# Optimization experiments

Hardware: AMD Instinct MI355X
Metric: run time of the kernel (lower is better)

The kernel has to match this reference:

```python
import jax, jax.numpy as jnp
import numpy as np

T0 = 0.0
T1 = 20.0
DT0 = 0.02
NT = 1000
N = 64
K = 8
N_ITS = 2


def _lininterp(tg, yg, t):
    # linear interpolation of grid values yg (len(tg), ...) at scalar t
    i = jnp.clip(jnp.searchsorted(tg, t, side='right') - 1, 0, tg.shape[0] - 2)
    w = jnp.clip((t - tg[i]) / (tg[i + 1] - tg[i]), 0.0, 1.0)
    return (1.0 - w) * yg[i] + w * yg[i + 1]


def _rk4(field, y0, t_start, dt, nsteps):
    # fixed-step RK4; returns trajectory of shape (nsteps+1, *y0.shape)
    def step(y, t):
        k1 = field(t, y)
        k2 = field(t + 0.5 * dt, y + 0.5 * dt * k1)
        k3 = field(t + 0.5 * dt, y + 0.5 * dt * k2)
        k4 = field(t + dt, y + dt * k3)
        y1 = y + (dt / 6.0) * (k1 + 2.0 * k2 + 2.0 * k3 + k4)
        return y1, y1
    tgrid = t_start + dt * jnp.arange(nsteps, dtype=y0.dtype)
    _, ys = jax.lax.scan(step, y0, tgrid)
    return jnp.concatenate([y0[None], ys], axis=0)


def setup_inputs() -> dict:
    key = jax.random.key(0)
    ks = jax.random.split(key, 5)
    n, k = N, K
    s = 1.0 / np.sqrt(n)
    A = 0.3 * s * jax.random.normal(ks[0], (n, n), jnp.float32) - 0.5 * jnp.eye(n, dtype=jnp.float32)
    B = s * jax.random.normal(ks[1], (n, k), jnp.float32)
    H = 0.1 * s * jax.random.normal(ks[2], (n, n, k), jnp.float32)
    Rm = jax.random.normal(ks[3], (k, k), jnp.float32)
    R = jnp.eye(k, dtype=jnp.float32) + 0.1 * (Rm @ Rm.T) / k
    Q = jnp.eye(n, dtype=jnp.float32)
    F = 0.5 * jnp.eye(n, dtype=jnp.float32)
    x0 = 0.5 * jax.random.normal(ks[4], (n, 1), jnp.float32)
    return {"F": F, "Q": Q, "R": R, "A": A, "B": B, "H": H, "x0": x0, "N_its": N_ITS}


def _solve(F, Q, R, A, B, H, x0, N_its):
    Ri = jnp.linalg.inv(R)
    dA = jnp.conj(A).T
    ts = T0 + DT0 * jnp.arange(NT, dtype=x0.dtype)              # state grid (excludes t1)
    tgP = T0 + DT0 * jnp.arange(NT + 1, dtype=x0.dtype)         # costate grid (includes t1)

    def A_k_tilde(pk):
        return A - 0.5 * (jnp.einsum('ijk,kl,ml,m->ij', H, Ri, B, pk)
                          + jnp.einsum('ir,rs,mjs,m->ij', B, Ri, H, pk))

    def B_k_tilde(xk):
        return B + jnp.einsum('jnl,n->jl', H, xk)

    def S_k_tilde(xk):
        Bt = B_k_tilde(xk)
        return (jnp.einsum('ik,kl,jl->ij', Bt, Ri, Bt)
                - 0.5 * (jnp.einsum('iqp,q,pr,jr->ij', H, xk, Ri, B)
                         + jnp.einsum('it,tv,jwv,w->ij', B, Ri, H, xk)))

    def Q_k_tilde(pk):
        return (jnp.einsum('m,mik,kl,njl,n->ij', pk, H, Ri, H, pk)
                + jnp.einsum('m,mjr,rs,nis,n->ij', pk, H, Ri, H, pk))

    def A_k(xk, pk, Pk):
        return A_k_tilde(pk) - S_k_tilde(xk) @ Pk

    def Q_k(xk, pk, Pk):
        return Q_k_tilde(pk) - Pk @ S_k_tilde(xk) @ Pk

    def u_k(xk, xk1, Pk1):
        return jnp.einsum('kl,jnl,n,jm,m->k', -Ri, H, xk, Pk1, xk1)

    # LQR Riccati, integrated backward from t1 with y(t1) = F
    def P_field(t, y):
        return -y @ A - dA @ y - Q + jnp.einsum('im,mk,kl,nl,nj->ij', y, B, Ri, B, y)
    Ps = jnp.flip(_rk4(P_field, F, T1, -DT0, NT), axis=0)        # (NT+1, n, n) on tgP
    P_of = lambda t: _lininterp(tgP, Ps, t)

    x_res = jnp.zeros((N_its + 1, NT, N), dtype=x0.dtype)
    u_res = jnp.zeros((N_its + 1, NT, K), dtype=x0.dtype)

    # iteration 0: no control
    x0_traj = _rk4(lambda t, y: A @ y, x0, T0, DT0, NT - 1)       # (NT, n, 1)
    x_res = x_res.at[0].set(x0_traj[:, :, 0])

    # iteration 1: LQR initial guess
    def init_field(t, y):
        return (A - jnp.einsum('ik,kl,nl,nj->ij', B, Ri, B, P_of(t))) @ y
    x_grid = _rk4(init_field, x0, T0, DT0, NT - 1)                # (NT, n, 1)
    x_res = x_res.at[1].set(x_grid[:, :, 0])
    u1 = jax.vmap(lambda Pt, xt: -jnp.einsum('kl,nl,nj,j->k', Ri, B, Pt, xt))(Ps[:NT], x_grid[:, :, 0])
    u_res = u_res.at[1].set(u1)

    P_grid = Ps
    for i in range(1, N_its):
        x_of = lambda t, xg=x_grid: _lininterp(ts, xg, t)[:, 0]
        Pc_of = lambda t, Pg=P_grid: _lininterp(tgP, Pg, t)

        def Akt_field(t, y, x_of=x_of, Pc_of=Pc_of):
            Pkt = Pc_of(t)
            xkt = x_of(t)
            pkt = Pkt @ xkt
            return A_k(xkt, pkt, Pkt) @ y

        x_k1 = _rk4(Akt_field, x0, T0, DT0, NT - 1)               # (NT, n, 1)

        def Pk1_field(t, y, x_of=x_of, Pc_of=Pc_of):
            Pkt = Pc_of(t)
            xkt = x_of(t)
            pkt = Pkt @ xkt
            Akt = A_k(xkt, pkt, Pkt)
            return -y @ Akt - Akt.T @ y - Q_k(xkt, pkt, Pkt)

        P_k1 = jnp.flip(_rk4(Pk1_field, F, T1, -DT0, NT), axis=0)  # (NT+1, n, n)

        u_grid = jax.vmap(u_k)(x_grid[:, :, 0], x_k1[:, :, 0], P_k1[:NT])  # (NT, k)
        u_of = lambda t, ug=u_grid: _lininterp(ts, ug, t)

        def eval_field(t, y, x_of=x_of, Pc_of=Pc_of, u_of=u_of):
            xkt = x_of(t)
            pkt = Pc_of(t) @ xkt
            return A_k_tilde(pkt) @ y + (B_k_tilde(xkt) @ u_of(t))[:, None]

        x_eval = _rk4(eval_field, x0, T0, DT0, NT - 1)            # (NT, n, 1)
        x_res = x_res.at[i + 1].set(x_eval[:, :, 0])
        u_res = u_res.at[i + 1].set(u_grid)
        x_grid = x_k1
        P_grid = P_k1
    return x_res, u_res


def reference(F, Q, R, A, B, H, x0, N_its):
    return _solve(F, Q, R, A, B, H, x0, int(N_its))
```

## Files before the change

kernel.cpp:

```cpp
#include <hip/hip_runtime.h>
#include <cmath>


#define NTS 1000
#define DT  0.02f
#define LDM 68

constexpr int O_PS   = 0;
constexpr int O_PK1  = O_PS  + (NTS+1)*4096;
constexpr int O_XG   = O_PK1 + NTS*4096;
constexpr int O_XK1  = O_XG  + NTS*64;
constexpr int O_H1   = O_XK1 + NTS*64;
constexpr int O_H2   = O_H1  + 64*8*64;
constexpr int O_RI   = O_H2  + 64*8*64;
constexpr int O_BRI  = O_RI  + 64;
constexpr int O_RIBT = O_BRI + 512;
constexpr int O_BT   = O_RIBT+ 512;
constexpr int WS_FLOATS = O_BT + 512;

constexpr int O_X0o = 0;
constexpr int O_X1o = 64000;
constexpr int O_X2o = 128000;
constexpr int O_U0o = 192000;
constexpr int O_U1o = 200000;
constexpr int O_U2o = 208000;

#define EW_FOR(I, J, IJ, ...) do { \
  const int _r = (int)threadIdx.x >> 2; const int _c0 = ((int)threadIdx.x & 3) << 4; \
  _Pragma("unroll") \
  for (int _e = 0; _e < 16; ++_e) { const int I = _r; const int J = _c0 + _e; const int IJ = (I)*LDM + (J); __VA_ARGS__; } \
} while (0)

__device__ __forceinline__ void ld4(float* d, const float* p) {
  const float4 v = *(const float4*)p; d[0]=v.x; d[1]=v.y; d[2]=v.z; d[3]=v.w;
}

template<int KD, int LDX, int LDY, int LDC, int OP>
__device__ __forceinline__ void mmNN(float* C, const float* X, const float* Y) {
  const int t = threadIdx.x;
  const int ti = (t >> 4) << 2, tj = (t & 15) << 2;
  float c[4][4] = {};
  #pragma unroll
  for (int m = 0; m < KD; m += 4) {
    float xv[4][4], yv[4][4];
    #pragma unroll
    for (int r = 0; r < 4; ++r) ld4(xv[r], &X[(ti + r) * LDX + m]);
    #pragma unroll
    for (int k = 0; k < 4; ++k) ld4(yv[k], &Y[(m + k) * LDY + tj]);
    #pragma unroll
    for (int r = 0; r < 4; ++r)
      #pragma unroll
      for (int k = 0; k < 4; ++k)
        #pragma unroll
        for (int j = 0; j < 4; ++j) c[r][j] += xv[r][k] * yv[k][j];
  }
  #pragma unroll
  for (int r = 0; r < 4; ++r) {
    float* dst = &C[(ti + r) * LDC + tj];
    #pragma unroll
    for (int j = 0; j < 4; ++j) {
      if (OP == 0) dst[j] = c[r][j];
      else if (OP == 1) dst[j] += c[r][j];
      else dst[j] -= c[r][j];
    }
  }
}

template<int KD, int LDX, int LDY, int LDC, int OP>
__device__ __forceinline__ void mmTN(float* C, const float* X, const float* Y) {
  const int t = threadIdx.x;
  const int ti = (t >> 4) << 2, tj = (t & 15) << 2;
  float c[4][4] = {};
  #pragma unroll
  for (int m = 0; m < KD; m += 4) {
    float xq[4][4], yv[4][4];
    #pragma unroll
    for (int k = 0; k < 4; ++k) ld4(xq[k], &X[(m + k) * LDX + ti]);
    #pragma unroll
    for (int k = 0; k < 4; ++k) ld4(yv[k], &Y[(m + k) * LDY + tj]);
    #pragma unroll
    for (int r = 0; r < 4; ++r)
      #pragma unroll
      for (int k = 0; k < 4; ++k)
        #pragma unroll
        for (int j = 0; j < 4; ++j) c[r][j] += xq[k][r] * yv[k][j];
  }
  #pragma unroll
  for (int r = 0; r < 4; ++r) {
    float* dst = &C[(ti + r) * LDC + tj];
    #pragma unroll
    for (int j = 0; j < 4; ++j) {
      if (OP == 0) dst[j] = c[r][j];
      else if (OP == 1) dst[j] += c[r][j];
      else dst[j] -= c[r][j];
    }
  }
}

template<int KD, int LDX, int LDYT, int LDC, int OP>
__device__ __forceinline__ void mmNT(float* C, const float* X, const float* Yt) {
  const int t = threadIdx.x;
  const int ti = (t >> 4) << 2, tj = (t & 15) << 2;
  float c[4][4] = {};
  #pragma unroll
  for (int m = 0; m < KD; m += 4) {
    float xv[4][4], yq[4][4];
    #pragma unroll
    for (int r = 0; r < 4; ++r) ld4(xv[r], &X[(ti + r) * LDX + m]);
    #pragma unroll
    for (int cc = 0; cc < 4; ++cc) ld4(yq[cc], &Yt[(tj + cc) * LDYT + m]);
    #pragma unroll
    for (int r = 0; r < 4; ++r)
      #pragma unroll
      for (int k = 0; k < 4; ++k)
        #pragma unroll
        for (int j = 0; j < 4; ++j) c[r][j] += xv[r][k] * yq[j][k];
  }
  #pragma unroll
  for (int r = 0; r < 4; ++r) {
    float* dst = &C[(ti + r) * LDC + tj];
    #pragma unroll
    for (int j = 0; j < 4; ++j) {
      if (OP == 0) dst[j] = c[r][j];
      else if (OP == 1) dst[j] += c[r][j];
      else dst[j] -= c[r][j];
    }
  }
}

__device__ __forceinline__ void mv64(float* out, const float* M, int ldm, const float* v, float* red) {
  const int t = threadIdx.x;
  const int r = t & 63, q = t >> 6, m0 = q << 4;
  float s = 0.f;
  #pragma unroll
  for (int m = 0; m < 16; ++m) s += M[r*ldm + m0 + m] * v[m0 + m];
  red[(q << 6) + r] = s;
  __syncthreads();
  if (t < 64) out[t] = (red[t] + red[64+t]) + (red[128+t] + red[192+t]);
  __syncthreads();
}

__device__ __forceinline__ void mv64_blend(float* out, const float* Ma, const float* Mb,
                                           float wa, float wb, const float* v, float* red) {
  const int t = threadIdx.x;
  const int r = t & 63, q = t >> 6, m0 = q << 4;
  float sa = 0.f, sb = 0.f;
  #pragma unroll
  for (int m = 0; m < 16; ++m) {
    const float vv = v[m0 + m];
    sa += Ma[r*64 + m0 + m] * vv;
    sb += Mb[r*64 + m0 + m] * vv;
  }
  red[(q << 6) + r] = wa*sa + wb*sb;
  __syncthreads();
  if (t < 64) out[t] = (red[t] + red[64+t]) + (red[128+t] + red[192+t]);
  __syncthreads();
}

__device__ __forceinline__ float dot64g(const float* __restrict__ a, const float* v) {
  float s = 0.f;
  #pragma unroll
  for (int m = 0; m < 64; m += 4) {
    const float4 av = *(const float4*)&a[m];
    s += av.x*v[m] + av.y*v[m+1] + av.z*v[m+2] + av.w*v[m+3];
  }
  return s;
}

__device__ __forceinline__ void interpIW(float t, int imax, int& i, float& w) {
  int ii = (int)floorf(t * 50.0f);
  ii = ii < 0 ? 0 : (ii > imax ? imax : ii);
  const float gi  = DT * (float)ii;
  const float gi1 = DT * (float)(ii + 1);
  float ww = (t - gi) / (gi1 - gi);
  ww = fminf(fmaxf(ww, 0.0f), 1.0f);
  i = ii; w = ww;
}

__global__ void kPrepA(const float* __restrict__ Rg, const float* __restrict__ Bg, float* __restrict__ ws) {
  __shared__ float M[8][17];
  __shared__ int spiv;
  const int t = threadIdx.x;
  if (t < 8) {
    #pragma unroll
    for (int c = 0; c < 8; ++c) { M[t][c] = Rg[t*8 + c]; M[t][8 + c] = (t == c) ? 1.0f : 0.0f; }
  }
  __syncthreads();
  for (int col = 0; col < 8; ++col) {
    if (t == 0) {
      int piv = col; float best = fabsf(M[col][col]);
      for (int r = col + 1; r < 8; ++r) { const float a = fabsf(M[r][col]); if (a > best) { best = a; piv = r; } }
      spiv = piv;
    }
    __syncthreads();
    const int piv = spiv;
    if (piv != col && t < 16) { const float tmp = M[col][t]; M[col][t] = M[piv][t]; M[piv][t] = tmp; }
    __syncthreads();
    if (t < 16) { const float pv = M[col][col]; M[col][t] = M[col][t] / pv; }
    __syncthreads();
    if (t < 8 && t != col) {
      const float f = M[t][col];
      #pragma unroll
      for (int c = 0; c < 16; ++c) M[t][c] -= f * M[col][c];
    }
    __syncthreads();
  }
  if (t < 64) ws[O_RI + t] = M[t >> 3][8 + (t & 7)];
  __syncthreads();
  for (int o = t; o < 512; o += 64) {
    const int i = o >> 3, l = o & 7;
    float s = 0.f;
    #pragma unroll
    for (int p = 0; p < 8; ++p) s += Bg[i*8 + p] * M[p][8 + l];
    ws[O_BRI + o] = s;
    const int p2 = o >> 6, j2 = o & 63;
    float s2 = 0.f;
    #pragma unroll
    for (int l2 = 0; l2 < 8; ++l2) s2 += M[p2][8 + l2] * Bg[j2*8 + l2];
    ws[O_RIBT + o] = s2;
    ws[O_BT + o] = Bg[j2*8 + p2];
  }
}

__global__ void kPrepB(const float* __restrict__ Hg, float* __restrict__ ws, float* __restrict__ out) {
  const int total = 32768 + 32768 + 8000;
  for (int idx = blockIdx.x * 256 + threadIdx.x; idx < total; idx += gridDim.x * 256) {
    if (idx < 32768) {
      const int j = idx >> 9, l = (idx >> 6) & 7, n = idx & 63;
      ws[O_H1 + idx] = Hg[j*512 + n*8 + l];
    } else if (idx < 65536) {
      const int k2 = idx - 32768;
      const int j = k2 >> 9, s = (k2 >> 6) & 7, m = k2 & 63;
      ws[O_H2 + k2] = Hg[m*512 + j*8 + s];
    } else {
      out[O_U0o + (idx - 65536)] = 0.0f;
    }
  }
}

__global__ void __launch_bounds__(256) kP(const float* __restrict__ Fg, const float* __restrict__ Qg,
                                          const float* __restrict__ Ag,
                                          const float* __restrict__ ws, float* __restrict__ Ps) {
  __shared__ float y0[64*LDM], acc[64*LDM], ytm[64*LDM], kb[64*LDM];
  __shared__ float As[64*LDM], ATs[64*LDM], Qs[64*LDM];
  __shared__ float BTs[512], Ris[64], yB[512], M2s[512], T8[8*LDM], red[256];
  const int t = threadIdx.x;
  { const int r = t >> 2, c0 = (t & 3) << 4;
    #pragma unroll
    for (int e = 0; e < 16; ++e) { const int c = c0 + e;
      y0[r*LDM + c]  = Fg[r*64 + c];
      As[r*LDM + c]  = Ag[r*64 + c];
      ATs[c*LDM + r] = Ag[r*64 + c];
      Qs[r*LDM + c]  = Qg[r*64 + c];
    } }
  for (int o = t; o < 512; o += 256) BTs[o] = ws[O_BT + o];
  if (t < 64) Ris[t] = ws[O_RI + t];
  __syncthreads();
  { const int r = t >> 2, c0 = (t & 3) << 4;
    #pragma unroll
    for (int e = 0; e < 16; ++e) Ps[(size_t)NTS*4096 + r*64 + c0 + e] = y0[r*LDM + c0 + e]; }

  const float dt = -DT;
  const float c16 = dt / 6.0f, c13 = 2.0f * c16, c12 = 0.5f * dt;

  auto field = [&](const float* src) {
    for (int o = t; o < 512; o += 256) {
      const int i = o >> 3, l = o & 7;
      const float* sr = &src[i*LDM];
      const float* br = &BTs[l*64];
      float s = 0.f;
      #pragma unroll
      for (int m = 0; m < 64; ++m) s += sr[m] * br[m];
      yB[o] = s;
    }
    __syncthreads();
    for (int o = t; o < 512; o += 256) {
      const int i = o >> 3, l = o & 7;
      float s = 0.f;
      #pragma unroll
      for (int p = 0; p < 8; ++p) s += yB[i*8 + p] * Ris[p*8 + l];
      M2s[o] = s;
    }
    for (int o = t; o < 512; o += 256) {
      const int p = o >> 6, jj = o & 63;
      const float* br = &BTs[p*64];
      float s = 0.f;
      #pragma unroll
      for (int m = 0; m < 64; ++m) s += br[m] * src[m*LDM + jj];
      T8[p*LDM + jj] = s;
    }
    __syncthreads();
    mmNN<8,  8,   LDM, LDM, 0>(kb, M2s, T8);
    mmNN<64, LDM, LDM, LDM, 2>(kb, src, As);
    mmNN<64, LDM, LDM, LDM, 2>(kb, ATs, src);
    __syncthreads();
  };

  for (int j = 0; j < NTS; ++j) {
    for (int st = 0; st < 4; ++st) {
      const float* src = (st == 0) ? y0 : ytm;
      field(src);
      EW_FOR(I, J, IJ, {
        const float kv = kb[IJ] - Qs[IJ];
        if (st == 0)      { acc[IJ] = y0[IJ] + c16*kv; ytm[IJ] = y0[IJ] + c12*kv; }
        else if (st == 1) { acc[IJ] += c13*kv;         ytm[IJ] = y0[IJ] + c12*kv; }
        else if (st == 2) { acc[IJ] += c13*kv;         ytm[IJ] = y0[IJ] + dt*kv;  }
        else              { y0[IJ] = acc[IJ] + c16*kv; }
      });
      __syncthreads();
    }
    { const int r = t >> 2, c0 = (t & 3) << 4;
      float4* dst = (float4*)&Ps[(size_t)(NTS-1-j)*4096 + r*64 + c0];
      #pragma unroll
      for (int e = 0; e < 4; ++e) {
        const float* s4 = &y0[r*LDM + c0 + 4*e];
        dst[e] = make_float4(s4[0], s4[1], s4[2], s4[3]);
      } }
    __syncthreads();
  }
}

__global__ void __launch_bounds__(256) kX0(const float* __restrict__ Ag, const float* __restrict__ x0g,
                                           float* __restrict__ out) {
  __shared__ float As[64*LDM], xv[64], xt[64], ks[4][64], red[256];
  const int t = threadIdx.x;
  { const int r = t >> 2, c0 = (t & 3) << 4;
    #pragma unroll
    for (int e = 0; e < 16; ++e) As[r*LDM + c0 + e] = Ag[r*64 + c0 + e]; }
  if (t < 64) xv[t] = x0g[t];
  __syncthreads();
  for (int j = 0; j < NTS; ++j) {
    if (t < 64) out[O_X0o + j*64 + t] = xv[t];
    __syncthreads();
    if (j == NTS - 1) break;
    for (int st = 0; st < 4; ++st) {
      const float* src = (st == 0) ? xv : xt;
      mv64(ks[st], As, LDM, src, red);
      if (t < 64 && st < 3) xt[t] = xv[t] + (st == 2 ? DT : 0.01f) * ks[st][t];
      __syncthreads();
    }
    if (t < 64) xv[t] += (DT/6.0f) * (ks[0][t] + 2.0f*ks[1][t] + 2.0f*ks[2][t] + ks[3][t]);
    __syncthreads();
  }
}

__global__ void __launch_bounds__(256) kXgrid(const float* __restrict__ Ag, const float* __restrict__ Bg,
                                              const float* __restrict__ x0g,
                                              float* __restrict__ ws, float* __restrict__ out) {
  __shared__ float As[64*LDM], Bs[512], RiBTs[512];
  __shared__ float xv[64], xt[64], ks[4][64], pv[64], g8[8], red[256];
  const int t = threadIdx.x;
  const float* Ps = ws + O_PS;
  { const int r = t >> 2, c0 = (t & 3) << 4;
    #pragma unroll
    for (int e = 0; e < 16; ++e) As[r*LDM + c0 + e] = Ag[r*64 + c0 + e]; }
  for (int o = t; o < 512; o += 256) { Bs[o] = Bg[o]; RiBTs[o] = ws[O_RIBT + o]; }
  if (t < 64) xv[t] = x0g[t];
  __syncthreads();

  auto field = [&](float tau, const float* src, float* kout) {
    int i; float w; interpIW(tau, NTS - 1, i, w);
    mv64_blend(pv, Ps + (size_t)i*4096, Ps + (size_t)(i+1)*4096, 1.0f - w, w, src, red);
    if (t < 8) {
      float s = 0.f;
      #pragma unroll
      for (int m = 0; m < 64; ++m) s += RiBTs[t*64 + m] * pv[m];
      g8[t] = s;
    }
    mv64(kout, As, LDM, src, red);
    if (t < 64) {
      float s = 0.f;
      #pragma unroll
      for (int p = 0; p < 8; ++p) s += Bs[t*8 + p] * g8[p];
      kout[t] -= s;
    }
    __syncthreads();
  };

  for (int j = 0; j < NTS; ++j) {
    if (t < 64) { out[O_X1o + j*64 + t] = xv[t]; ws[O_XG + j*64 + t] = xv[t]; }
    mv64(pv, Ps + (size_t)j*4096, 64, xv, red);
    if (t < 8) {
      float s = 0.f;
      #pragma unroll
      for (int m = 0; m < 64; ++m) s += RiBTs[t*64 + m] * pv[m];
      out[O_U1o + j*8 + t] = -s;
    }
    __syncthreads();
    if (j == NTS - 1) break;
    const float tj = DT * (float)j;
    for (int st = 0; st < 4; ++st) {
      const float tau = tj + ((st == 0) ? 0.0f : (st == 3) ? DT : 0.01f);
      const float* src = (st == 0) ? xv : xt;
      field(tau, src, ks[st]);
      if (t < 64 && st < 3) xt[t] = xv[t] + (st == 2 ? DT : 0.01f) * ks[st][t];
      __syncthreads();
    }
    if (t < 64) xv[t] += (DT/6.0f) * (ks[0][t] + 2.0f*ks[1][t] + 2.0f*ks[2][t] + ks[3][t]);
    __syncthreads();
  }
}

__global__ void __launch_bounds__(256) kXk1(const float* __restrict__ Ag, const float* __restrict__ Bg,
                                            const float* __restrict__ Hg, const float* __restrict__ x0g,
                                            float* __restrict__ ws) {
  __shared__ float Atil[64*LDM];
  __shared__ float Bs[512], BTs[512], RiBTs[512], BRis[512], Ris[64];
  __shared__ float Hx[512], Bt[512], BtRi[512], G[512];
  __shared__ float xv[64], xt[64], xk[64], pk[64], pv[64], sv[64];
  __shared__ float ks[4][64], e1[8], e2[8], e3[8], e8v[8], w8[8], red[256];
  __shared__ int ci; __shared__ float cw;
  const int t = threadIdx.x;
  const float* Ps = ws + O_PS;
  const float* xg = ws + O_XG;
  for (int o = t; o < 512; o += 256) {
    Bs[o] = Bg[o]; BTs[o] = ws[O_BT + o]; RiBTs[o] = ws[O_RIBT + o]; BRis[o] = ws[O_BRI + o];
  }
  if (t < 64) { Ris[t] = ws[O_RI + t]; xv[t] = x0g[t]; }
  __syncthreads();

  auto build = [&](float tau) {
    int i, ix; float w, wx;
    interpIW(tau, NTS - 1, i, w);
    interpIW(tau, NTS - 2, ix, wx);
    if (t == 0) { ci = i; cw = w; }
    if (t < 64) xk[t] = (1.0f - wx) * xg[ix*64 + t] + wx * xg[(ix+1)*64 + t];
    __syncthreads();
    mv64_blend(pk, Ps + (size_t)i*4096, Ps + (size_t)(i+1)*4096, 1.0f - w, w, xk, red);
    if (t < 8) {
      float s = 0.f;
      #pragma unroll
      for (int m = 0; m < 64; ++m) s += BTs[t*64 + m] * pk[m];
      e8v[t] = s;
    }
    __syncthreads();
    if (t < 8) {
      float s = 0.f;
      #pragma unroll
      for (int l = 0; l < 8; ++l) s += Ris[t*8 + l] * e8v[l];
      w8[t] = s;
    }
    for (int o = t; o < 512; o += 256) {
      const float hx = dot64g(&ws[O_H1 + o*64], xk);
      Hx[o] = hx; Bt[o] = Bs[o] + hx;
      G[o]  = dot64g(&ws[O_H2 + o*64], pk);
    }
    __syncthreads();
    for (int o = t; o < 512; o += 256) {
      const int i2 = o >> 3, l = o & 7;
      float s = 0.f;
      #pragma unroll
      for (int p = 0; p < 8; ++p) s += Bt[i2*8 + p] * Ris[p*8 + l];
      BtRi[o] = s;
    }
    EW_FOR(I, J, IJ, {
      const float4 h0 = *(const float4*)&Hg[I*512 + J*8];
      const float4 h1 = *(const float4*)&Hg[I*512 + J*8 + 4];
      Atil[IJ] = h0.x*w8[0]+h0.y*w8[1]+h0.z*w8[2]+h0.w*w8[3]
               + h1.x*w8[4]+h1.y*w8[5]+h1.z*w8[6]+h1.w*w8[7];
    });
    __syncthreads();
    mmNT<8, 8, 8, LDM, 1>(Atil, BRis, G);
    __syncthreads();
    EW_FOR(I, J, IJ, { Atil[IJ] = Ag[I*64 + J] - 0.5f*Atil[IJ]; });
    __syncthreads();
  };

  auto fieldK = [&](const float* src, float* kout) {
    mv64_blend(pv, Ps + (size_t)ci*4096, Ps + (size_t)(ci+1)*4096, 1.0f - cw, cw, src, red);
    if (t < 8) {
      float s = 0.f;
      #pragma unroll
      for (int m = 0; m < 64; ++m) s += Bt[m*8 + t] * pv[m];
      e1[t] = s;
    } else if (t < 16) {
      const int l = t - 8; float s = 0.f;
      #pragma unroll
      for (int m = 0; m < 64; ++m) s += RiBTs[l*64 + m] * pv[m];
      e2[l] = s;
    } else if (t < 24) {
      const int l = t - 16; float s = 0.f;
      #pragma unroll
      for (int m = 0; m < 64; ++m) s += Hx[m*8 + l] * pv[m];
      e3[l] = s;
    }
    __syncthreads();
    if (t < 64) {
      float s1 = 0.f, s2 = 0.f, s3 = 0.f;
      #pragma unroll
      for (int p = 0; p < 8; ++p) {
        s1 += BtRi[t*8 + p] * e1[p];
        s2 += Hx[t*8 + p]   * e2[p];
        s3 += BRis[t*8 + p] * e3[p];
      }
      sv[t] = s1 - 0.5f*(s2 + s3);
    }
    mv64(kout, Atil, LDM, src, red);
    if (t < 64) kout[t] -= sv[t];
    __syncthreads();
  };

  for (int j = 0; j < NTS; ++j) {
    if (t < 64) ws[O_XK1 + j*64 + t] = xv[t];
    __syncthreads();
    if (j == NTS - 1) break;
    const float tj = DT * (float)j;
    for (int st = 0; st < 4; ++st) {
      if (st != 2) build(tj + ((st == 0) ? 0.0f : (st == 3) ? DT : 0.01f));
      const float* src = (st == 0) ? xv : xt;
      fieldK(src, ks[st]);
      if (t < 64 && st < 3) xt[t] = xv[t] + (st == 2 ? DT : 0.01f) * ks[st][t];
      __syncthreads();
    }
    if (t < 64) xv[t] += (DT/6.0f) * (ks[0][t] + 2.0f*ks[1][t] + 2.0f*ks[2][t] + ks[3][t]);
    __syncthreads();
  }
}

__global__ void __launch_bounds__(256) kPk1(const float* __restrict__ Fg, const float* __restrict__ Ag,
                                            const float* __restrict__ Bg, const float* __restrict__ Hg,
                                            float* __restrict__ ws) {
  __shared__ float y0[64*LDM], acc[64*LDM], ytm[64*LDM], kb[64*LDM];
  __shared__ float Pc[64*LDM], Ss[64*LDM], SP[64*LDM], Akt[64*LDM];
  __shared__ float Bs[512], BTs[512], RiBTs[512], BRis[512], Ris[64];
  __shared__ float Hx[512], Bt[512], BtRi[512], G[512], GRi[512];
  __shared__ float xk[64], pk[64], e8v[8], w8[8], red[256];
  const int t = threadIdx.x;
  const float* Ps = ws + O_PS;
  const float* xg = ws + O_XG;
  float* Pk1g = ws + O_PK1;
  { const int r = t >> 2, c0 = (t & 3) << 4;
    #pragma unroll
    for (int e = 0; e < 16; ++e) y0[r*LDM + c0 + e] = Fg[r*64 + c0 + e]; }
  for (int o = t; o < 512; o += 256) {
    Bs[o] = Bg[o]; BTs[o] = ws[O_BT + o]; RiBTs[o] = ws[O_RIBT + o]; BRis[o] = ws[O_BRI + o];
  }
  if (t < 64) Ris[t] = ws[O_RI + t];
  __syncthreads();

  const float dt = -DT;
  const float c16 = dt / 6.0f, c13 = 2.0f * c16, c12 = 0.5f * dt;

  auto build = [&](float tau) {
    int i, ix; float w, wx;
    interpIW(tau, NTS - 1, i, w);
    interpIW(tau, NTS - 2, ix, wx);
    if (t < 64) xk[t] = (1.0f - wx) * xg[ix*64 + t] + wx * xg[(ix+1)*64 + t];
    { const int r = t >> 2, c0 = (t & 3) << 4;
      const float4* pa = (const float4*)&Ps[(size_t)i*4096 + r*64 + c0];
      const float4* pb = (const float4*)&Ps[(size_t)(i+1)*4096 + r*64 + c0];
      const float wa = 1.0f - w;
      #pragma unroll
      for (int e = 0; e < 4; ++e) {
        const float4 a = pa[e], b = pb[e];
        float* d = &Pc[r*LDM + c0 + 4*e];
        d[0] = wa*a.x + w*b.x; d[1] = wa*a.y + w*b.y; d[2] = wa*a.z + w*b.z; d[3] = wa*a.w + w*b.w;
      } }
    __syncthreads();
    mv64(pk, Pc, LDM, xk, red);
    if (t < 8) {
      float s = 0.f;
      #pragma unroll
      for (int m = 0; m < 64; ++m) s += BTs[t*64 + m] * pk[m];
      e8v[t] = s;
    }
    __syncthreads();
    if (t < 8) {
      float s = 0.f;
      #pragma unroll
      for (int l = 0; l < 8; ++l) s += Ris[t*8 + l] * e8v[l];
      w8[t] = s;
    }
    for (int o = t; o < 512; o += 256) {
      const float hx = dot64g(&ws[O_H1 + o*64], xk);
      Hx[o] = hx; Bt[o] = Bs[o] + hx;
      G[o]  = dot64g(&ws[O_H2 + o*64], pk);
    }
    __syncthreads();
    for (int o = t; o < 512; o += 256) {
      const int i2 = o >> 3, l = o & 7;
      float s1 = 0.f, s2 = 0.f;
      #pragma unroll
      for (int p = 0; p < 8; ++p) { s1 += Bt[i2*8 + p] * Ris[p*8 + l]; s2 += G[i2*8 + p] * Ris[p*8 + l]; }
      BtRi[o] = s1; GRi[o] = s2;
    }
    __syncthreads();
    mmNN<8, 8, 64, LDM, 0>(kb, Hx, RiBTs);
    mmNT<8, 8, 8,  LDM, 0>(Ss, BtRi, Bt);
    __syncthreads();
    EW_FOR(I, J, IJ, { Ss[IJ] = Ss[IJ] - 0.5f*(kb[IJ] + kb[J*LDM + I]); });
    __syncthreads();
    mmNN<64, LDM, LDM, LDM, 0>(SP, Ss, Pc);
    __syncthreads();
    mmNN<64, LDM, LDM, LDM, 0>(kb, Pc, SP);
    mmNT<8, 8, 8, LDM, 0>(Ss, GRi, G);
    __syncthreads();
    EW_FOR(I, J, IJ, {
      Pc[IJ] = Ss[IJ] + Ss[J*LDM + I] - kb[IJ];
      const float4 h0 = *(const float4*)&Hg[I*512 + J*8];
      const float4 h1 = *(const float4*)&Hg[I*512 + J*8 + 4];
      Akt[IJ] = h0.x*w8[0]+h0.y*w8[1]+h0.z*w8[2]+h0.w*w8[3]
              + h1.x*w8[4]+h1.y*w8[5]+h1.z*w8[6]+h1.w*w8[7];
    });
    __syncthreads();
    mmNT<8, 8, 8, LDM, 1>(Akt, BRis, G);
    __syncthreads();
    EW_FOR(I, J, IJ, { Akt[IJ] = Ag[I*64 + J] - 0.5f*Akt[IJ] - SP[IJ]; });
    __syncthreads();
  };

  auto evalf = [&](const float* src) {
    mmNN<64, LDM, LDM, LDM, 0>(kb, src, Akt);
    mmTN<64, LDM, LDM, LDM, 1>(kb, Akt, src);
    __syncthreads();
  };

  for (int j = 0; j < NTS; ++j) {
    const float tj = 20.0f - DT * (float)j;
    for (int st = 0; st < 4; ++st) {
      if (st != 2) build(tj - ((st == 0) ? 0.0f : (st == 3) ? DT : 0.01f));
      const float* src = (st == 0) ? y0 : ytm;
      evalf(src);
      EW_FOR(I, J, IJ, {
        const float kv = -(kb[IJ] + Pc[IJ]);
        if (st == 0)      { acc[IJ] = y0[IJ] + c16*kv; ytm[IJ] = y0[IJ] + c12*kv; }
        else if (st == 1) { acc[IJ] += c13*kv;         ytm[IJ] = y0[IJ] + c12*kv; }
        else if (st == 2) { acc[IJ] += c13*kv;         ytm[IJ] = y0[IJ] + dt*kv;  }
        else              { y0[IJ] = acc[IJ] + c16*kv; }
      });
      __syncthreads();
    }
    { const int r = t >> 2, c0 = (t & 3) << 4;
      float4* dst = (float4*)&Pk1g[(size_t)(NTS-1-j)*4096 + r*64 + c0];
      #pragma unroll
      for (int e = 0; e < 4; ++e) {
        const float* s4 = &y0[r*LDM + c0 + 4*e];
        dst[e] = make_float4(s4[0], s4[1], s4[2], s4[3]);
      } }
    __syncthreads();
  }
}

__global__ void __launch_bounds__(256) kUgrid(const float* __restrict__ ws, float* __restrict__ out) {
  const int j = blockIdx.x, t = threadIdx.x;
  __shared__ float xvj[64], x1[64], vv[64], hxv[512], w8s[8], Ris[64], red[256];
  if (t < 64) { xvj[t] = ws[O_XG + j*64 + t]; x1[t] = ws[O_XK1 + j*64 + t]; Ris[t] = ws[O_RI + t]; }
  __syncthreads();
  mv64(vv, ws + O_PK1 + (size_t)j*4096, 64, x1, red);
  for (int o = t; o < 512; o += 256) {
    const int j2 = o >> 3;
    hxv[o] = vv[j2] * dot64g(&ws[O_H1 + o*64], xvj);
  }
  __syncthreads();
  if (t < 8) {
    float s = 0.f;
    #pragma unroll
    for (int j2 = 0; j2 < 64; ++j2) s += hxv[j2*8 + t];
    w8s[t] = s;
  }
  __syncthreads();
  if (t < 8) {
    float s = 0.f;
    #pragma unroll
    for (int l = 0; l < 8; ++l) s += Ris[t*8 + l] * w8s[l];
    out[O_U2o + j*8 + t] = -s;
  }
}

__global__ void __launch_bounds__(256) kXeval(const float* __restrict__ Ag, const float* __restrict__ Bg,
                                              const float* __restrict__ Hg, const float* __restrict__ x0g,
                                              float* __restrict__ ws, float* __restrict__ out) {
  __shared__ float Atil[64*LDM];
  __shared__ float Bs[512], BTs[512], BRis[512], Ris[64];
  __shared__ float Hx[512], Bt[512], G[512];
  __shared__ float xv[64], xt[64], xk[64], pk[64], bu[64];
  __shared__ float ks[4][64], e8v[8], w8[8], uu8[8], red[256];
  const int t = threadIdx.x;
  const float* Ps = ws + O_PS;
  const float* xg = ws + O_XG;
  const float* Ug = out + O_U2o;
  for (int o = t; o < 512; o += 256) { Bs[o] = Bg[o]; BTs[o] = ws[O_BT + o]; BRis[o] = ws[O_BRI + o]; }
  if (t < 64) { Ris[t] = ws[O_RI + t]; xv[t] = x0g[t]; }
  __syncthreads();

  auto build = [&](float tau) {
    int i, ix; float w, wx;
    interpIW(tau, NTS - 1, i, w);
    interpIW(tau, NTS - 2, ix, wx);
    if (t < 64) xk[t] = (1.0f - wx) * xg[ix*64 + t] + wx * xg[(ix+1)*64 + t];
    __syncthreads();
    mv64_blend(pk, Ps + (size_t)i*4096, Ps + (size_t)(i+1)*4096, 1.0f - w, w, xk, red);
    if (t < 8) {
      float s = 0.f;
      #pragma unroll
      for (int m = 0; m < 64; ++m) s += BTs[t*64 + m] * pk[m];
      e8v[t] = s;
    }
    __syncthreads();
    if (t < 8) {
      float s = 0.f;
      #pragma unroll
      for (int l = 0; l < 8; ++l) s += Ris[t*8 + l] * e8v[l];
      w8[t] = s;
    }
    for (int o = t; o < 512; o += 256) {
      const float hx = dot64g(&ws[O_H1 + o*64], xk);
      Hx[o] = hx; Bt[o] = Bs[o] + hx;
      G[o]  = dot64g(&ws[O_H2 + o*64], pk);
    }
    __syncthreads();
    EW_FOR(I, J, IJ, {
      const float4 h0 = *(const float4*)&Hg[I*512 + J*8];
      const float4 h1 = *(const float4*)&Hg[I*512 + J*8 + 4];
      Atil[IJ] = h0.x*w8[0]+h0.y*w8[1]+h0.z*w8[2]+h0.w*w8[3]
               + h1.x*w8[4]+h1.y*w8[5]+h1.z*w8[6]+h1.w*w8[7];
    });
    __syncthreads();
    mmNT<8, 8, 8, LDM, 1>(Atil, BRis, G);
    __syncthreads();
    EW_FOR(I, J, IJ, { Atil[IJ] = Ag[I*64 + J] - 0.5f*Atil[IJ]; });
    if (t < 8) uu8[t] = (1.0f - wx) * Ug[ix*8 + t] + wx * Ug[(ix+1)*8 + t];
    __syncthreads();
    if (t < 64) {
      float s = 0.f;
      #pragma unroll
      for (int l = 0; l < 8; ++l) s += Bt[t*8 + l] * uu8[l];
      bu[t] = s;
    }
    __syncthreads();
  };

  auto fieldE = [&](const float* src, float* kout) {
    mv64(kout, Atil, LDM, src, red);
    if (t < 64) kout[t] += bu[t];
    __syncthreads();
  };

  for (int j = 0; j < NTS; ++j) {
    if (t < 64) out[O_X2o + j*64 + t] = xv[t];
    __syncthreads();
    if (j == NTS - 1) break;
    const float tj = DT * (float)j;
    for (int st = 0; st < 4; ++st) {
      if (st != 2) build(tj + ((st == 0) ? 0.0f : (st == 3) ? DT : 0.01f));
      const float* src = (st == 0) ? xv : xt;
      fieldE(src, ks[st]);
      if (t < 64 && st < 3) xt[t] = xv[t] + (st == 2 ? DT : 0.01f) * ks[st][t];
      __syncthreads();
    }
    if (t < 64) xv[t] += (DT/6.0f) * (ks[0][t] + 2.0f*ks[1][t] + 2.0f*ks[2][t] + ks[3][t]);
    __syncthreads();
  }
}

extern "C" void kernel_launch(void* const* d_in, const int* in_sizes, int n_in,
                              void* d_out, int out_size, void* d_ws, size_t ws_size,
                              hipStream_t stream) {
  const float* F  = (const float*)d_in[0];
  const float* Q  = (const float*)d_in[1];
  const float* R  = (const float*)d_in[2];
  const float* A  = (const float*)d_in[3];
  const float* B  = (const float*)d_in[4];
  const float* H  = (const float*)d_in[5];
  const float* x0 = (const float*)d_in[6];
  float* out = (float*)d_out;
  float* ws  = (float*)d_ws;
  (void)in_sizes; (void)n_in; (void)out_size; (void)ws_size;

  kPrepA<<<1, 64, 0, stream>>>(R, B, ws);
  kPrepB<<<96, 256, 0, stream>>>(H, ws, out);
  kP<<<1, 256, 0, stream>>>(F, Q, A, ws, ws + O_PS);
  kX0<<<1, 256, 0, stream>>>(A, x0, out);
  kXgrid<<<1, 256, 0, stream>>>(A, B, x0, ws, out);
  kXk1<<<1, 256, 0, stream>>>(A, B, H, x0, ws);
  kPk1<<<1, 256, 0, stream>>>(F, A, B, H, ws);
  kUgrid<<<NTS, 256, 0, stream>>>(ws, out);
  kXeval<<<1, 256, 0, stream>>>(A, B, H, x0, ws, out);
}
```

Before: 229.5 ms.

## Widen sequential RK4 kernels to 1024 threads and exploit symmetry in Riccati fields

```diff
diff --git a/kernel.cpp b/kernel.cpp
--- a/kernel.cpp
+++ b/kernel.cpp
@@ -10,13 +10,11 @@
 constexpr int O_PK1  = O_PS  + (NTS+1)*4096;
 constexpr int O_XG   = O_PK1 + NTS*4096;
 constexpr int O_XK1  = O_XG  + NTS*64;
-constexpr int O_H1   = O_XK1 + NTS*64;
-constexpr int O_H2   = O_H1  + 64*8*64;
-constexpr int O_RI   = O_H2  + 64*8*64;
+constexpr int O_H1T  = O_XK1 + NTS*64;
+constexpr int O_RI   = O_H1T + 64*512;
 constexpr int O_BRI  = O_RI  + 64;
 constexpr int O_RIBT = O_BRI + 512;
 constexpr int O_BT   = O_RIBT+ 512;
-constexpr int WS_FLOATS = O_BT + 512;
 
 constexpr int O_X0o = 0;
 constexpr int O_X1o = 64000;
@@ -25,146 +23,134 @@
 constexpr int O_U1o = 200000;
 constexpr int O_U2o = 208000;
 
-#define EW_FOR(I, J, IJ, ...) do { \
-  const int _r = (int)threadIdx.x >> 2; const int _c0 = ((int)threadIdx.x & 3) << 4; \
+#define EW4(I, J, IJ, ...) do { \
+  const int _r = (int)threadIdx.x >> 4; const int _c0 = ((int)threadIdx.x & 15) << 2; \
   _Pragma("unroll") \
-  for (int _e = 0; _e < 16; ++_e) { const int I = _r; const int J = _c0 + _e; const int IJ = (I)*LDM + (J); __VA_ARGS__; } \
+  for (int _e = 0; _e < 4; ++_e) { const int I = _r; const int J = _c0 + _e; const int IJ = (I)*LDM + (J); __VA_ARGS__; } \
 } while (0)
 
-__device__ __forceinline__ void ld4(float* d, const float* p) {
-  const float4 v = *(const float4*)p; d[0]=v.x; d[1]=v.y; d[2]=v.z; d[3]=v.w;
+__device__ __forceinline__ float wred64(float v) {
+  v += __shfl_down(v, 32, 64);
+  v += __shfl_down(v, 16, 64);
+  v += __shfl_down(v, 8, 64);
+  v += __shfl_down(v, 4, 64);
+  v += __shfl_down(v, 2, 64);
+  v += __shfl_down(v, 1, 64);
+  return v;
 }
 
 template<int KD, int LDX, int LDY, int LDC, int OP>
 __device__ __forceinline__ void mmNN(float* C, const float* X, const float* Y) {
   const int t = threadIdx.x;
-  const int ti = (t >> 4) << 2, tj = (t & 15) << 2;
-  float c[4][4] = {};
+  const int row = t >> 4, tj = (t & 15) << 2;
+  float c0 = 0.f, c1 = 0.f, c2 = 0.f, c3 = 0.f;
   #pragma unroll
   for (int m = 0; m < KD; m += 4) {
-    float xv[4][4], yv[4][4];
-    #pragma unroll
-    for (int r = 0; r < 4; ++r) ld4(xv[r], &X[(ti + r) * LDX + m]);
-    #pragma unroll
-    for (int k = 0; k < 4; ++k) ld4(yv[k], &Y[(m + k) * LDY + tj]);
-    #pragma unroll
-    for (int r = 0; r < 4; ++r)
-      #pragma unroll
-      for (int k = 0; k < 4; ++k)
-        #pragma unroll
-        for (int j = 0; j < 4; ++j) c[r][j] += xv[r][k] * yv[k][j];
-  }
-  #pragma unroll
-  for (int r = 0; r < 4; ++r) {
-    float* dst = &C[(ti + r) * LDC + tj];
-    #pragma unroll
-    for (int j = 0; j < 4; ++j) {
-      if (OP == 0) dst[j] = c[r][j];
-      else if (OP == 1) dst[j] += c[r][j];
-      else dst[j] -= c[r][j];
-    }
-  }
-}
-
-template<int KD, int LDX, int LDY, int LDC, int OP>
-__device__ __forceinline__ void mmTN(float* C, const float* X, const float* Y) {
-  const int t = threadIdx.x;
-  const int ti = (t >> 4) << 2, tj = (t & 15) << 2;
-  float c[4][4] = {};
+    const float4 x4 = *(const float4*)&X[row*LDX + m];
+    const float4 ya = *(const float4*)&Y[(m+0)*LDY + tj];
+    const float4 yb = *(const float4*)&Y[(m+1)*LDY + tj];
+    const float4 yc = *(const float4*)&Y[(m+2)*LDY + tj];
+    const float4 yd = *(const float4*)&Y[(m+3)*LDY + tj];
+    c0 += x4.x*ya.x + x4.y*yb.x + x4.z*yc.x + x4.w*yd.x;
+    c1 += x4.x*ya.y + x4.y*yb.y + x4.z*yc.y + x4.w*yd.y;
+    c2 += x4.x*ya.z + x4.y*yb.z + x4.z*yc.z + x4.w*yd.z;
+    c3 += x4.x*ya.w + x4.y*yb.w + x4.z*yc.w + x4.w*yd.w;
+  }
+  float* dst = &C[row*LDC + tj];
+  if (OP == 0)      { dst[0] = c0; dst[1] = c1; dst[2] = c2; dst[3] = c3; }
+  else if (OP == 1) { dst[0] += c0; dst[1] += c1; dst[2] += c2; dst[3] += c3; }
+  else              { dst[0] -= c0; dst[1] -= c1; dst[2] -= c2; dst[3] -= c3; }
+}
+
+template<int KD, int LDX, int LDYT, int LDC, int OP>
+__device__ __forceinline__ void mmNT(float* C, const float* X, const float* Yt) {
+  const int t = threadIdx.x;
+  const int row = t >> 4, tj = (t & 15) << 2;
+  float c[4] = {0.f, 0.f, 0.f, 0.f};
   #pragma unroll
   for (int m = 0; m < KD; m += 4) {
-    float xq[4][4], yv[4][4];
-    #pragma unroll
-    for (int k = 0; k < 4; ++k) ld4(xq[k], &X[(m + k) * LDX + ti]);
-    #pragma unroll
-    for (int k = 0; k < 4; ++k) ld4(yv[k], &Y[(m + k) * LDY + tj]);
-    #pragma unroll
-    for (int r = 0; r < 4; ++r)
-      #pragma unroll
-      for (int k = 0; k < 4; ++k)
-        #pragma unroll
-        for (int j = 0; j < 4; ++j) c[r][j] += xq[k][r] * yv[k][j];
-  }
+    const float4 x4 = *(const float4*)&X[row*LDX + m];
+    #pragma unroll
+    for (int j = 0; j < 4; ++j) {
+      const float4 y4 = *(const float4*)&Yt[(tj+j)*LDYT + m];
+      c[j] += x4.x*y4.x + x4.y*y4.y + x4.z*y4.z + x4.w*y4.w;
+    }
+  }
+  float* dst = &C[row*LDC + tj];
   #pragma unroll
-  for (int r = 0; r < 4; ++r) {
-    float* dst = &C[(ti + r) * LDC + tj];
-    #pragma unroll
-    for (int j = 0; j < 4; ++j) {
-      if (OP == 0) dst[j] = c[r][j];
-      else if (OP == 1) dst[j] += c[r][j];
-      else dst[j] -= c[r][j];
-    }
-  }
-}
-
-template<int KD, int LDX, int LDYT, int LDC, int OP>
-__device__ __forceinline__ void mmNT(float* C, const float* X, const float* Yt) {
-  const int t = threadIdx.x;
-  const int ti = (t >> 4) << 2, tj = (t & 15) << 2;
-  float c[4][4] = {};
-  #pragma unroll
-  for (int m = 0; m < KD; m += 4) {
-    float xv[4][4], yq[4][4];
-    #pragma unroll
-    for (int r = 0; r < 4; ++r) ld4(xv[r], &X[(ti + r) * LDX + m]);
-    #pragma unroll
-    for (int cc = 0; cc < 4; ++cc) ld4(yq[cc], &Yt[(tj + cc) * LDYT + m]);
-    #pragma unroll
-    for (int r = 0; r < 4; ++r)
-      #pragma unroll
-      for (int k = 0; k < 4; ++k)
-        #pragma unroll
-        for (int j = 0; j < 4; ++j) c[r][j] += xv[r][k] * yq[j][k];
-  }
-  #pragma unroll
-  for (int r = 0; r < 4; ++r) {
-    float* dst = &C[(ti + r) * LDC + tj];
-    #pragma unroll
-    for (int j = 0; j < 4; ++j) {
-      if (OP == 0) dst[j] = c[r][j];
-      else if (OP == 1) dst[j] += c[r][j];
-      else dst[j] -= c[r][j];
-    }
-  }
-}
-
-__device__ __forceinline__ void mv64(float* out, const float* M, int ldm, const float* v, float* red) {
-  const int t = threadIdx.x;
-  const int r = t & 63, q = t >> 6, m0 = q << 4;
+  for (int j = 0; j < 4; ++j) {
+    if (OP == 0) dst[j] = c[j];
+    else if (OP == 1) dst[j] += c[j];
+    else dst[j] -= c[j];
+  }
+}
+
+__device__ __forceinline__ void mvL(float* out, const float* M, const float* v, float* red) {
+  const int t = threadIdx.x, r = t & 63, m0 = (t >> 6) << 2;
+  float s = M[r*LDM+m0]*v[m0] + M[r*LDM+m0+1]*v[m0+1]
+          + M[r*LDM+m0+2]*v[m0+2] + M[r*LDM+m0+3]*v[m0+3];
+  red[t] = s;
+  __syncthreads();
+  if (t < 64) {
+    float a = 0.f;
+    #pragma unroll
+    for (int q = 0; q < 16; ++q) a += red[q*64 + t];
+    out[t] = a;
+  }
+  __syncthreads();
+}
+
+__device__ __forceinline__ void mvLsym(float* out, const float* M, const float* v, float* red) {
+  const int t = threadIdx.x, r = t & 63, m0 = (t >> 6) << 2;
   float s = 0.f;
   #pragma unroll
-  for (int m = 0; m < 16; ++m) s += M[r*ldm + m0 + m] * v[m0 + m];
-  red[(q << 6) + r] = s;
-  __syncthreads();
-  if (t < 64) out[t] = (red[t] + red[64+t]) + (red[128+t] + red[192+t]);
-  __syncthreads();
-}
-
-__device__ __forceinline__ void mv64_blend(float* out, const float* Ma, const float* Mb,
-                                           float wa, float wb, const float* v, float* red) {
-  const int t = threadIdx.x;
-  const int r = t & 63, q = t >> 6, m0 = q << 4;
+  for (int k = 0; k < 4; ++k) s += M[(m0+k)*LDM + r] * v[m0+k];
+  red[t] = s;
+  __syncthreads();
+  if (t < 64) {
+    float a = 0.f;
+    #pragma unroll
+    for (int q = 0; q < 16; ++q) a += red[q*64 + t];
+    out[t] = a;
+  }
+  __syncthreads();
+}
+
+__device__ __forceinline__ void mvG(float* out, const float* __restrict__ Mg, const float* v, float* red) {
+  const int t = threadIdx.x, r = t & 63, m0 = (t >> 6) << 2;
+  float s = 0.f;
+  #pragma unroll
+  for (int k = 0; k < 4; ++k) s += Mg[(m0+k)*64 + r] * v[m0+k];
+  red[t] = s;
+  __syncthreads();
+  if (t < 64) {
+    float a = 0.f;
+    #pragma unroll
+    for (int q = 0; q < 16; ++q) a += red[q*64 + t];
+    out[t] = a;
+  }
+  __syncthreads();
+}
+
+__device__ __forceinline__ void mvGb(float* out, const float* __restrict__ Ma, const float* __restrict__ Mb,
+                                     float wa, float wb, const float* v, float* red) {
+  const int t = threadIdx.x, r = t & 63, m0 = (t >> 6) << 2;
   float sa = 0.f, sb = 0.f;
   #pragma unroll
-  for (int m = 0; m < 16; ++m) {
-    const float vv = v[m0 + m];
-    sa += Ma[r*64 + m0 + m] * vv;
-    sb += Mb[r*64 + m0 + m] * vv;
-  }
-  red[(q << 6) + r] = wa*sa + wb*sb;
-  __syncthreads();
-  if (t < 64) out[t] = (red[t] + red[64+t]) + (red[128+t] + red[192+t]);
-  __syncthreads();
-}
-
-__device__ __forceinline__ float dot64g(const float* __restrict__ a, const float* v) {
-  float s = 0.f;
-  #pragma unroll
-  for (int m = 0; m < 64; m += 4) {
-    const float4 av = *(const float4*)&a[m];
-    s += av.x*v[m] + av.y*v[m+1] + av.z*v[m+2] + av.w*v[m+3];
-  }
-  return s;
+  for (int k = 0; k < 4; ++k) {
+    const float vv = v[m0+k];
+    sa += Ma[(m0+k)*64 + r] * vv;
+    sb += Mb[(m0+k)*64 + r] * vv;
+  }
+  red[t] = wa*sa + wb*sb;
+  __syncthreads();
+  if (t < 64) {
+    float a = 0.f;
+    #pragma unroll
+    for (int q = 0; q < 16; ++q) a += red[q*64 + t];
+    out[t] = a;
+  }
+  __syncthreads();
 }
 
 __device__ __forceinline__ void interpIW(float t, int imax, int& i, float& w) {
@@ -223,76 +209,59 @@
 }
 
 __global__ void kPrepB(const float* __restrict__ Hg, float* __restrict__ ws, float* __restrict__ out) {
-  const int total = 32768 + 32768 + 8000;
+  const int total = 32768 + 8000;
   for (int idx = blockIdx.x * 256 + threadIdx.x; idx < total; idx += gridDim.x * 256) {
     if (idx < 32768) {
-      const int j = idx >> 9, l = (idx >> 6) & 7, n = idx & 63;
-      ws[O_H1 + idx] = Hg[j*512 + n*8 + l];
-    } else if (idx < 65536) {
-      const int k2 = idx - 32768;
-      const int j = k2 >> 9, s = (k2 >> 6) & 7, m = k2 & 63;
-      ws[O_H2 + k2] = Hg[m*512 + j*8 + s];
+      const int n = idx >> 9, o = idx & 511, j = o >> 3, l = o & 7;
+      ws[O_H1T + idx] = Hg[j*512 + n*8 + l];
     } else {
-      out[O_U0o + (idx - 65536)] = 0.0f;
-    }
-  }
-}
-
-__global__ void __launch_bounds__(256) kP(const float* __restrict__ Fg, const float* __restrict__ Qg,
-                                          const float* __restrict__ Ag,
-                                          const float* __restrict__ ws, float* __restrict__ Ps) {
-  __shared__ float y0[64*LDM], acc[64*LDM], ytm[64*LDM], kb[64*LDM];
-  __shared__ float As[64*LDM], ATs[64*LDM], Qs[64*LDM];
-  __shared__ float BTs[512], Ris[64], yB[512], M2s[512], T8[8*LDM], red[256];
-  const int t = threadIdx.x;
-  { const int r = t >> 2, c0 = (t & 3) << 4;
-    #pragma unroll
-    for (int e = 0; e < 16; ++e) { const int c = c0 + e;
-      y0[r*LDM + c]  = Fg[r*64 + c];
-      As[r*LDM + c]  = Ag[r*64 + c];
-      ATs[c*LDM + r] = Ag[r*64 + c];
-      Qs[r*LDM + c]  = Qg[r*64 + c];
+      out[O_U0o + (idx - 32768)] = 0.0f;
+    }
+  }
+}
+
+__global__ void __launch_bounds__(1024) kP(const float* __restrict__ Fg, const float* __restrict__ Qg,
+                                           const float* __restrict__ Ag,
+                                           const float* __restrict__ ws, float* __restrict__ Ps) {
+  __shared__ float y0[64*LDM], acc[64*LDM], ytm[64*LDM], kb[64*LDM], Ms[64*LDM], As[64*LDM], Qs[64*LDM];
+  __shared__ float BTs[512], Ris[64], yB[512], M2s[512], red[1024];
+  const int t = threadIdx.x;
+  { const int r = t >> 4, c0 = (t & 15) << 2;
+    #pragma unroll
+    for (int e = 0; e < 4; ++e) { const int c = c0 + e;
+      y0[r*LDM + c] = Fg[r*64 + c];
+      As[r*LDM + c] = Ag[r*64 + c];
+      Qs[r*LDM + c] = Qg[r*64 + c];
     } }
-  for (int o = t; o < 512; o += 256) BTs[o] = ws[O_BT + o];
+  if (t < 512) BTs[t] = ws[O_BT + t];
   if (t < 64) Ris[t] = ws[O_RI + t];
   __syncthreads();
-  { const int r = t >> 2, c0 = (t & 3) << 4;
-    #pragma unroll
-    for (int e = 0; e < 16; ++e) Ps[(size_t)NTS*4096 + r*64 + c0 + e] = y0[r*LDM + c0 + e]; }
+  { const int r = t >> 4, c0 = (t & 15) << 2;
+    #pragma unroll
+    for (int e = 0; e < 4; ++e) Ps[(size_t)NTS*4096 + r*64 + c0 + e] = y0[r*LDM + c0 + e]; }
 
   const float dt = -DT;
   const float c16 = dt / 6.0f, c13 = 2.0f * c16, c12 = 0.5f * dt;
 
   auto field = [&](const float* src) {
-    for (int o = t; o < 512; o += 256) {
-      const int i = o >> 3, l = o & 7;
-      const float* sr = &src[i*LDM];
-      const float* br = &BTs[l*64];
-      float s = 0.f;
-      #pragma unroll
-      for (int m = 0; m < 64; ++m) s += sr[m] * br[m];
-      yB[o] = s;
-    }
-    __syncthreads();
-    for (int o = t; o < 512; o += 256) {
-      const int i = o >> 3, l = o & 7;
+    { const int i = t & 63, l = (t >> 6) & 7, mb = (t >> 9) << 5;
+      float s = 0.f;
+      #pragma unroll 8
+      for (int m = 0; m < 32; ++m) s += src[(mb+m)*LDM + i] * BTs[l*64 + mb + m];
+      red[t] = s; }
+    __syncthreads();
+    if (t < 512) { const int i = t & 63, l = t >> 6; yB[i*8 + l] = red[t] + red[t + 512]; }
+    __syncthreads();
+    if (t < 512) {
+      const int i = t >> 3, l = t & 7;
       float s = 0.f;
       #pragma unroll
       for (int p = 0; p < 8; ++p) s += yB[i*8 + p] * Ris[p*8 + l];
-      M2s[o] = s;
-    }
-    for (int o = t; o < 512; o += 256) {
-      const int p = o >> 6, jj = o & 63;
-      const float* br = &BTs[p*64];
-      float s = 0.f;
-      #pragma unroll
-      for (int m = 0; m < 64; ++m) s += br[m] * src[m*LDM + jj];
-      T8[p*LDM + jj] = s;
-    }
-    __syncthreads();
-    mmNN<8,  8,   LDM, LDM, 0>(kb, M2s, T8);
-    mmNN<64, LDM, LDM, LDM, 2>(kb, src, As);
-    mmNN<64, LDM, LDM, LDM, 2>(kb, ATs, src);
+      M2s[t] = s;
+    }
+    __syncthreads();
+    mmNT<8, 8, 8, LDM, 0>(kb, M2s, yB);
+    mmNN<64, LDM, LDM, LDM, 0>(Ms, src, As);
     __syncthreads();
   };
 
@@ -300,8 +269,8 @@
     for (int st = 0; st < 4; ++st) {
       const float* src = (st == 0) ? y0 : ytm;
       field(src);
-      EW_FOR(I, J, IJ, {
-        const float kv = kb[IJ] - Qs[IJ];
+      EW4(I, J, IJ, {
+        const float kv = kb[IJ] - Ms[IJ] - Ms[J*LDM + I] - Qs[IJ];
         if (st == 0)      { acc[IJ] = y0[IJ] + c16*kv; ytm[IJ] = y0[IJ] + c12*kv; }
         else if (st == 1) { acc[IJ] += c13*kv;         ytm[IJ] = y0[IJ] + c12*kv; }
         else if (st == 2) { acc[IJ] += c13*kv;         ytm[IJ] = y0[IJ] + dt*kv;  }
@@ -309,24 +278,20 @@
       });
       __syncthreads();
     }
-    { const int r = t >> 2, c0 = (t & 3) << 4;
+    { const int r = t >> 4, c0 = (t & 15) << 2;
       float4* dst = (float4*)&Ps[(size_t)(NTS-1-j)*4096 + r*64 + c0];
-      #pragma unroll
-      for (int e = 0; e < 4; ++e) {
-        const float* s4 = &y0[r*LDM + c0 + 4*e];
-        dst[e] = make_float4(s4[0], s4[1], s4[2], s4[3]);
-      } }
-    __syncthreads();
-  }
-}
-
-__global__ void __launch_bounds__(256) kX0(const float* __restrict__ Ag, const float* __restrict__ x0g,
-                                           float* __restrict__ out) {
-  __shared__ float As[64*LDM], xv[64], xt[64], ks[4][64], red[256];
-  const int t = threadIdx.x;
-  { const int r = t >> 2, c0 = (t & 3) << 4;
-    #pragma unroll
-    for (int e = 0; e < 16; ++e) As[r*LDM + c0 + e] = Ag[r*64 + c0 + e]; }
+      *dst = make_float4(y0[r*LDM+c0], y0[r*LDM+c0+1], y0[r*LDM+c0+2], y0[r*LDM+c0+3]); }
+    __syncthreads();
+  }
+}
+
+__global__ void __launch_bounds__(1024) kX0(const float* __restrict__ Ag, const float* __restrict__ x0g,
+                                            float* __restrict__ out) {
+  __shared__ float As[64*LDM], xv[64], xt[64], ks[4][64], red[1024];
+  const int t = threadIdx.x;
+  { const int r = t >> 4, c0 = (t & 15) << 2;
+    #pragma unroll
+    for (int e = 0; e < 4; ++e) As[r*LDM + c0 + e] = Ag[r*64 + c0 + e]; }
   if (t < 64) xv[t] = x0g[t];
   __syncthreads();
   for (int j = 0; j < NTS; ++j) {
@@ -335,7 +300,7 @@
     if (j == NTS - 1) break;
     for (int st = 0; st < 4; ++st) {
       const float* src = (st == 0) ? xv : xt;
-      mv64(ks[st], As, LDM, src, red);
+      mvL(ks[st], As, src, red);
       if (t < 64 && st < 3) xt[t] = xv[t] + (st == 2 ? DT : 0.01f) * ks[st][t];
       __syncthreads();
     }
@@ -344,30 +309,26 @@
   }
 }
 
-__global__ void __launch_bounds__(256) kXgrid(const float* __restrict__ Ag, const float* __restrict__ Bg,
-                                              const float* __restrict__ x0g,
-                                              float* __restrict__ ws, float* __restrict__ out) {
+__global__ void __launch_bounds__(1024) kXgrid(const float* __restrict__ Ag, const float* __restrict__ Bg,
+                                               const float* __restrict__ x0g,
+                                               float* __restrict__ ws, float* __restrict__ out) {
   __shared__ float As[64*LDM], Bs[512], RiBTs[512];
-  __shared__ float xv[64], xt[64], ks[4][64], pv[64], g8[8], red[256];
+  __shared__ float xv[64], xt[64], ks[4][64], pv[64], g8[8], red[1024];
   const int t = threadIdx.x;
   const float* Ps = ws + O_PS;
-  { const int r = t >> 2, c0 = (t & 3) << 4;
-    #pragma unroll
-    for (int e = 0; e < 16; ++e) As[r*LDM + c0 + e] = Ag[r*64 + c0 + e]; }
-  for (int o = t; o < 512; o += 256) { Bs[o] = Bg[o]; RiBTs[o] = ws[O_RIBT + o]; }
+  { const int r = t >> 4, c0 = (t & 15) << 2;
+    #pragma unroll
+    for (int e = 0; e < 4; ++e) As[r*LDM + c0 + e] = Ag[r*64 + c0 + e]; }
+  if (t < 512) { Bs[t] = Bg[t]; RiBTs[t] = ws[O_RIBT + t]; }
   if (t < 64) xv[t] = x0g[t];
   __syncthreads();
 
   auto field = [&](float tau, const float* src, float* kout) {
     int i; float w; interpIW(tau, NTS - 1, i, w);
-    mv64_blend(pv, Ps + (size_t)i*4096, Ps + (size_t)(i+1)*4096, 1.0f - w, w, src, red);
-    if (t < 8) {
-      float s = 0.f;
-      #pragma unroll
-      for (int m = 0; m < 64; ++m) s += RiBTs[t*64 + m] * pv[m];
-      g8[t] = s;
-    }
-    mv64(kout, As, LDM, src, red);
+    mvGb(pv, Ps + (size_t)i*4096, Ps + (size_t)(i+1)*4096, 1.0f - w, w, src, red);
+    { const int wv = t >> 6, m = t & 63;
+      if (wv < 8) { const float rr = wred64(RiBTs[wv*64 + m] * pv[m]); if (m == 0) g8[wv] = rr; } }
+    mvL(kout, As, src, red);
     if (t < 64) {
       float s = 0.f;
       #pragma unroll
@@ -379,10 +340,11 @@
 
   for (int j = 0; j < NTS; ++j) {
     if (t < 64) { out[O_X1o + j*64 + t] = xv[t]; ws[O_XG + j*64 + t] = xv[t]; }
-    mv64(pv, Ps + (size_t)j*4096, 64, xv, red);
+    __syncthreads();
+    mvG(pv, Ps + (size_t)j*4096, xv, red);
     if (t < 8) {
       float s = 0.f;
-      #pragma unroll
+      #pragma unroll 8
       for (int m = 0; m < 64; ++m) s += RiBTs[t*64 + m] * pv[m];
       out[O_U1o + j*8 + t] = -s;
     }
@@ -401,21 +363,19 @@
   }
 }
 
-__global__ void __launch_bounds__(256) kXk1(const float* __restrict__ Ag, const float* __restrict__ Bg,
-                                            const float* __restrict__ Hg, const float* __restrict__ x0g,
-                                            float* __restrict__ ws) {
+__global__ void __launch_bounds__(1024) kXk1(const float* __restrict__ Ag, const float* __restrict__ Bg,
+                                             const float* __restrict__ Hg, const float* __restrict__ x0g,
+                                             float* __restrict__ ws) {
   __shared__ float Atil[64*LDM];
-  __shared__ float Bs[512], BTs[512], RiBTs[512], BRis[512], Ris[64];
+  __shared__ float RiBTs[512], BRis[512], Ris[64];
   __shared__ float Hx[512], Bt[512], BtRi[512], G[512];
   __shared__ float xv[64], xt[64], xk[64], pk[64], pv[64], sv[64];
-  __shared__ float ks[4][64], e1[8], e2[8], e3[8], e8v[8], w8[8], red[256];
+  __shared__ float ks[4][64], e1[8], e2[8], e3[8], e8v[8], w8[8], red[1024];
   __shared__ int ci; __shared__ float cw;
   const int t = threadIdx.x;
   const float* Ps = ws + O_PS;
   const float* xg = ws + O_XG;
-  for (int o = t; o < 512; o += 256) {
-    Bs[o] = Bg[o]; BTs[o] = ws[O_BT + o]; RiBTs[o] = ws[O_RIBT + o]; BRis[o] = ws[O_BRI + o];
-  }
+  if (t < 512) { RiBTs[t] = ws[O_RIBT + t]; BRis[t] = ws[O_BRI + t]; }
   if (t < 64) { Ris[t] = ws[O_RI + t]; xv[t] = x0g[t]; }
   __syncthreads();
 
@@ -426,13 +386,21 @@
     if (t == 0) { ci = i; cw = w; }
     if (t < 64) xk[t] = (1.0f - wx) * xg[ix*64 + t] + wx * xg[(ix+1)*64 + t];
     __syncthreads();
-    mv64_blend(pk, Ps + (size_t)i*4096, Ps + (size_t)(i+1)*4096, 1.0f - w, w, xk, red);
-    if (t < 8) {
-      float s = 0.f;
-      #pragma unroll
-      for (int m = 0; m < 64; ++m) s += BTs[t*64 + m] * pk[m];
-      e8v[t] = s;
-    }
+    mvGb(pk, Ps + (size_t)i*4096, Ps + (size_t)(i+1)*4096, 1.0f - w, w, xk, red);
+    if (t < 512) {
+      const int o = t; float s = 0.f;
+      #pragma unroll 8
+      for (int n = 0; n < 64; ++n) s += ws[O_H1T + n*512 + o] * xk[n];
+      Hx[o] = s; Bt[o] = Bg[o] + s;
+    } else {
+      const int o = t - 512; float s = 0.f;
+      #pragma unroll 8
+      for (int m = 0; m < 64; ++m) s += Hg[m*512 + o] * pk[m];
+      G[o] = s;
+    }
+    __syncthreads();
+    { const int wv = t >> 6, m = t & 63;
+      if (wv < 8) { const float rr = wred64(ws[O_BT + wv*64 + m] * pk[m]); if (m == 0) e8v[wv] = rr; } }
     __syncthreads();
     if (t < 8) {
       float s = 0.f;
@@ -440,20 +408,15 @@
       for (int l = 0; l < 8; ++l) s += Ris[t*8 + l] * e8v[l];
       w8[t] = s;
     }
-    for (int o = t; o < 512; o += 256) {
-      const float hx = dot64g(&ws[O_H1 + o*64], xk);
-      Hx[o] = hx; Bt[o] = Bs[o] + hx;
-      G[o]  = dot64g(&ws[O_H2 + o*64], pk);
-    }
-    __syncthreads();
-    for (int o = t; o < 512; o += 256) {
-      const int i2 = o >> 3, l = o & 7;
+    __syncthreads();
+    if (t < 512) {
+      const int i2 = t >> 3, l = t & 7;
       float s = 0.f;
       #pragma unroll
       for (int p = 0; p < 8; ++p) s += Bt[i2*8 + p] * Ris[p*8 + l];
-      BtRi[o] = s;
-    }
-    EW_FOR(I, J, IJ, {
+      BtRi[t] = s;
+    }
+    EW4(I, J, IJ, {
       const float4 h0 = *(const float4*)&Hg[I*512 + J*8];
       const float4 h1 = *(const float4*)&Hg[I*512 + J*8 + 4];
       Atil[IJ] = h0.x*w8[0]+h0.y*w8[1]+h0.z*w8[2]+h0.w*w8[3]
@@ -462,28 +425,17 @@
     __syncthreads();
     mmNT<8, 8, 8, LDM, 1>(Atil, BRis, G);
     __syncthreads();
-    EW_FOR(I, J, IJ, { Atil[IJ] = Ag[I*64 + J] - 0.5f*Atil[IJ]; });
+    EW4(I, J, IJ, { Atil[IJ] = Ag[I*64 + J] - 0.5f*Atil[IJ]; });
     __syncthreads();
   };
 
   auto fieldK = [&](const float* src, float* kout) {
-    mv64_blend(pv, Ps + (size_t)ci*4096, Ps + (size_t)(ci+1)*4096, 1.0f - cw, cw, src, red);
-    if (t < 8) {
-      float s = 0.f;
-      #pragma unroll
-      for (int m = 0; m < 64; ++m) s += Bt[m*8 + t] * pv[m];
-      e1[t] = s;
-    } else if (t < 16) {
-      const int l = t - 8; float s = 0.f;
-      #pragma unroll
-      for (int m = 0; m < 64; ++m) s += RiBTs[l*64 + m] * pv[m];
-      e2[l] = s;
-    } else if (t < 24) {
-      const int l = t - 16; float s = 0.f;
-      #pragma unroll
-      for (int m = 0; m < 64; ++m) s += Hx[m*8 + l] * pv[m];
-      e3[l] = s;
-    }
+    mvGb(pv, Ps + (size_t)ci*4096, Ps + (size_t)(ci+1)*4096, 1.0f - cw, cw, src, red);
+    { const int wv = t >> 6, m = t & 63;
+      const float c1 = (wv < 8) ? Bt[m*8 + wv] * pv[m] : RiBTs[(wv-8)*64 + m] * pv[m];
+      const float r1 = wred64(c1);
+      if (m == 0) { if (wv < 8) e1[wv] = r1; else e2[wv-8] = r1; }
+      if (wv < 8) { const float r3 = wred64(Hx[m*8 + wv] * pv[m]); if (m == 0) e3[wv] = r3; } }
     __syncthreads();
     if (t < 64) {
       float s1 = 0.f, s2 = 0.f, s3 = 0.f;
@@ -495,7 +447,7 @@
       }
       sv[t] = s1 - 0.5f*(s2 + s3);
     }
-    mv64(kout, Atil, LDM, src, red);
+    mvL(kout, Atil, src, red);
     if (t < 64) kout[t] -= sv[t];
     __syncthreads();
   };
@@ -517,24 +469,22 @@
   }
 }
 
-__global__ void __launch_bounds__(256) kPk1(const float* __restrict__ Fg, const float* __restrict__ Ag,
-                                            const float* __restrict__ Bg, const float* __restrict__ Hg,
-                                            float* __restrict__ ws) {
+__global__ void __launch_bounds__(1024) kPk1(const float* __restrict__ Fg, const float* __restrict__ Ag,
+                                             const float* __restrict__ Bg, const float* __restrict__ Hg,
+                                             float* __restrict__ ws) {
   __shared__ float y0[64*LDM], acc[64*LDM], ytm[64*LDM], kb[64*LDM];
   __shared__ float Pc[64*LDM], Ss[64*LDM], SP[64*LDM], Akt[64*LDM];
-  __shared__ float Bs[512], BTs[512], RiBTs[512], BRis[512], Ris[64];
+  __shared__ float RiBTs[512], BRis[512], Ris[64];
   __shared__ float Hx[512], Bt[512], BtRi[512], G[512], GRi[512];
-  __shared__ float xk[64], pk[64], e8v[8], w8[8], red[256];
-  const int t = threadIdx.x;
-  const float* Ps = ws + O_PS;
+  __shared__ float xk[64], pk[64], e8v[8], w8[8], red[1024];
+  const int t = threadIdx.x;
+  const float* Psg = ws + O_PS;
   const float* xg = ws + O_XG;
   float* Pk1g = ws + O_PK1;
-  { const int r = t >> 2, c0 = (t & 3) << 4;
-    #pragma unroll
-    for (int e = 0; e < 16; ++e) y0[r*LDM + c0 + e] = Fg[r*64 + c0 + e]; }
-  for (int o = t; o < 512; o += 256) {
-    Bs[o] = Bg[o]; BTs[o] = ws[O_BT + o]; RiBTs[o] = ws[O_RIBT + o]; BRis[o] = ws[O_BRI + o];
-  }
+  { const int r = t >> 4, c0 = (t & 15) << 2;
+    #pragma unroll
+    for (int e = 0; e < 4; ++e) y0[r*LDM + c0 + e] = Fg[r*64 + c0 + e]; }
+  if (t < 512) { RiBTs[t] = ws[O_RIBT + t]; BRis[t] = ws[O_BRI + t]; }
   if (t < 64) Ris[t] = ws[O_RI + t];
   __syncthreads();
 
@@ -546,24 +496,28 @@
     interpIW(tau, NTS - 1, i, w);
     interpIW(tau, NTS - 2, ix, wx);
     if (t < 64) xk[t] = (1.0f - wx) * xg[ix*64 + t] + wx * xg[(ix+1)*64 + t];
-    { const int r = t >> 2, c0 = (t & 3) << 4;
-      const float4* pa = (const float4*)&Ps[(size_t)i*4096 + r*64 + c0];
-      const float4* pb = (const float4*)&Ps[(size_t)(i+1)*4096 + r*64 + c0];
+    { const int r = t >> 4, c0 = (t & 15) << 2;
+      const float4 a = *(const float4*)&Psg[(size_t)i*4096 + r*64 + c0];
+      const float4 b = *(const float4*)&Psg[(size_t)(i+1)*4096 + r*64 + c0];
       const float wa = 1.0f - w;
-      #pragma unroll
-      for (int e = 0; e < 4; ++e) {
-        const float4 a = pa[e], b = pb[e];
-        float* d = &Pc[r*LDM + c0 + 4*e];
-        d[0] = wa*a.x + w*b.x; d[1] = wa*a.y + w*b.y; d[2] = wa*a.z + w*b.z; d[3] = wa*a.w + w*b.w;
-      } }
-    __syncthreads();
-    mv64(pk, Pc, LDM, xk, red);
-    if (t < 8) {
-      float s = 0.f;
-      #pragma unroll
-      for (int m = 0; m < 64; ++m) s += BTs[t*64 + m] * pk[m];
-      e8v[t] = s;
-    }
+      float* d = &Pc[r*LDM + c0];
+      d[0] = wa*a.x + w*b.x; d[1] = wa*a.y + w*b.y; d[2] = wa*a.z + w*b.z; d[3] = wa*a.w + w*b.w; }
+    __syncthreads();
+    mvLsym(pk, Pc, xk, red);
+    if (t < 512) {
+      const int o = t; float s = 0.f;
+      #pragma unroll 8
+      for (int n = 0; n < 64; ++n) s += ws[O_H1T + n*512 + o] * xk[n];
+      Hx[o] = s; Bt[o] = Bg[o] + s;
+    } else {
+      const int o = t - 512; float s = 0.f;
+      #pragma unroll 8
+      for (int m = 0; m < 64; ++m) s += Hg[m*512 + o] * pk[m];
+      G[o] = s;
+    }
+    __syncthreads();
+    { const int wv = t >> 6, m = t & 63;
+      if (wv < 8) { const float rr = wred64(ws[O_BT + wv*64 + m] * pk[m]); if (m == 0) e8v[wv] = rr; } }
     __syncthreads();
     if (t < 8) {
       float s = 0.f;
@@ -571,47 +525,36 @@
       for (int l = 0; l < 8; ++l) s += Ris[t*8 + l] * e8v[l];
       w8[t] = s;
     }
-    for (int o = t; o < 512; o += 256) {
-      const float hx = dot64g(&ws[O_H1 + o*64], xk);
-      Hx[o] = hx; Bt[o] = Bs[o] + hx;
-      G[o]  = dot64g(&ws[O_H2 + o*64], pk);
-    }
-    __syncthreads();
-    for (int o = t; o < 512; o += 256) {
-      const int i2 = o >> 3, l = o & 7;
+    __syncthreads();
+    if (t < 512) {
+      const int i2 = t >> 3, l = t & 7;
       float s1 = 0.f, s2 = 0.f;
       #pragma unroll
       for (int p = 0; p < 8; ++p) { s1 += Bt[i2*8 + p] * Ris[p*8 + l]; s2 += G[i2*8 + p] * Ris[p*8 + l]; }
-      BtRi[o] = s1; GRi[o] = s2;
-    }
-    __syncthreads();
-    mmNN<8, 8, 64, LDM, 0>(kb, Hx, RiBTs);
-    mmNT<8, 8, 8,  LDM, 0>(Ss, BtRi, Bt);
-    __syncthreads();
-    EW_FOR(I, J, IJ, { Ss[IJ] = Ss[IJ] - 0.5f*(kb[IJ] + kb[J*LDM + I]); });
-    __syncthreads();
-    mmNN<64, LDM, LDM, LDM, 0>(SP, Ss, Pc);
-    __syncthreads();
-    mmNN<64, LDM, LDM, LDM, 0>(kb, Pc, SP);
-    mmNT<8, 8, 8, LDM, 0>(Ss, GRi, G);
-    __syncthreads();
-    EW_FOR(I, J, IJ, {
-      Pc[IJ] = Ss[IJ] + Ss[J*LDM + I] - kb[IJ];
+      BtRi[t] = s1; GRi[t] = s2;
+    }
+    EW4(I, J, IJ, {
       const float4 h0 = *(const float4*)&Hg[I*512 + J*8];
       const float4 h1 = *(const float4*)&Hg[I*512 + J*8 + 4];
       Akt[IJ] = h0.x*w8[0]+h0.y*w8[1]+h0.z*w8[2]+h0.w*w8[3]
               + h1.x*w8[4]+h1.y*w8[5]+h1.z*w8[6]+h1.w*w8[7];
     });
     __syncthreads();
+    mmNT<8, 8, 8, LDM, 0>(Ss, BtRi, Bt);
+    mmNN<8, 8, 64, LDM, 0>(kb, Hx, RiBTs);
+    __syncthreads();
+    EW4(I, J, IJ, { Ss[IJ] = Ss[IJ] - 0.5f*(kb[IJ] + kb[J*LDM + I]); });
+    __syncthreads();
+    mmNN<64, LDM, LDM, LDM, 0>(SP, Ss, Pc);
+    __syncthreads();
+    mmNN<64, LDM, LDM, LDM, 0>(kb, Pc, SP);
+    mmNT<8, 8, 8, LDM, 0>(Ss, GRi, G);
+    __syncthreads();
+    EW4(I, J, IJ, { Pc[IJ] = Ss[IJ] + Ss[J*LDM + I] - kb[IJ]; });
+    __syncthreads();
     mmNT<8, 8, 8, LDM, 1>(Akt, BRis, G);
     __syncthreads();
-    EW_FOR(I, J, IJ, { Akt[IJ] = Ag[I*64 + J] - 0.5f*Akt[IJ] - SP[IJ]; });
-    __syncthreads();
-  };
-
-  auto evalf = [&](const float* src) {
-    mmNN<64, LDM, LDM, LDM, 0>(kb, src, Akt);
-    mmTN<64, LDM, LDM, LDM, 1>(kb, Akt, src);
+    EW4(I, J, IJ, { Akt[IJ] = Ag[I*64 + J] - 0.5f*Akt[IJ] - SP[IJ]; });
     __syncthreads();
   };
 
@@ -620,9 +563,10 @@
     for (int st = 0; st < 4; ++st) {
       if (st != 2) build(tj - ((st == 0) ? 0.0f : (st == 3) ? DT : 0.01f));
       const float* src = (st == 0) ? y0 : ytm;
-      evalf(src);
-      EW_FOR(I, J, IJ, {
-        const float kv = -(kb[IJ] + Pc[IJ]);
+      mmNN<64, LDM, LDM, LDM, 0>(kb, src, Akt);
+      __syncthreads();
+      EW4(I, J, IJ, {
+        const float kv = -(kb[IJ] + kb[J*LDM + I] + Pc[IJ]);
         if (st == 0)      { acc[IJ] = y0[IJ] + c16*kv; ytm[IJ] = y0[IJ] + c12*kv; }
         else if (st == 1) { acc[IJ] += c13*kv;         ytm[IJ] = y0[IJ] + c12*kv; }
         else if (st == 2) { acc[IJ] += c13*kv;         ytm[IJ] = y0[IJ] + dt*kv;  }
@@ -630,31 +574,37 @@
       });
       __syncthreads();
     }
-    { const int r = t >> 2, c0 = (t & 3) << 4;
+    { const int r = t >> 4, c0 = (t & 15) << 2;
       float4* dst = (float4*)&Pk1g[(size_t)(NTS-1-j)*4096 + r*64 + c0];
-      #pragma unroll
-      for (int e = 0; e < 4; ++e) {
-        const float* s4 = &y0[r*LDM + c0 + 4*e];
-        dst[e] = make_float4(s4[0], s4[1], s4[2], s4[3]);
-      } }
+      *dst = make_float4(y0[r*LDM+c0], y0[r*LDM+c0+1], y0[r*LDM+c0+2], y0[r*LDM+c0+3]); }
     __syncthreads();
   }
 }
 
 __global__ void __launch_bounds__(256) kUgrid(const float* __restrict__ ws, float* __restrict__ out) {
   const int j = blockIdx.x, t = threadIdx.x;
-  __shared__ float xvj[64], x1[64], vv[64], hxv[512], w8s[8], Ris[64], red[256];
-  if (t < 64) { xvj[t] = ws[O_XG + j*64 + t]; x1[t] = ws[O_XK1 + j*64 + t]; Ris[t] = ws[O_RI + t]; }
-  __syncthreads();
-  mv64(vv, ws + O_PK1 + (size_t)j*4096, 64, x1, red);
+  __shared__ float xvj[64], x1[64], vv[64], hxv[512], w8s[8], red[256];
+  if (t < 64) { xvj[t] = ws[O_XG + j*64 + t]; x1[t] = ws[O_XK1 + j*64 + t]; }
+  __syncthreads();
+  { const int r = t & 63, m0 = (t >> 6) << 4;
+    const float* Mg = ws + O_PK1 + (size_t)j*4096;
+    float s = 0.f;
+    #pragma unroll
+    for (int m = 0; m < 16; ++m) s += Mg[(m0+m)*64 + r] * x1[m0+m];
+    red[t] = s; }
+  __syncthreads();
+  if (t < 64) vv[t] = (red[t] + red[64+t]) + (red[128+t] + red[192+t]);
+  __syncthreads();
   for (int o = t; o < 512; o += 256) {
-    const int j2 = o >> 3;
-    hxv[o] = vv[j2] * dot64g(&ws[O_H1 + o*64], xvj);
+    float s = 0.f;
+    #pragma unroll 8
+    for (int n = 0; n < 64; ++n) s += ws[O_H1T + n*512 + o] * xvj[n];
+    hxv[o] = vv[o >> 3] * s;
   }
   __syncthreads();
   if (t < 8) {
     float s = 0.f;
-    #pragma unroll
+    #pragma unroll 8
     for (int j2 = 0; j2 < 64; ++j2) s += hxv[j2*8 + t];
     w8s[t] = s;
   }
@@ -662,24 +612,24 @@
   if (t < 8) {
     float s = 0.f;
     #pragma unroll
-    for (int l = 0; l < 8; ++l) s += Ris[t*8 + l] * w8s[l];
+    for (int l = 0; l < 8; ++l) s += ws[O_RI + t*8 + l] * w8s[l];
     out[O_U2o + j*8 + t] = -s;
   }
 }
 
-__global__ void __launch_bounds__(256) kXeval(const float* __restrict__ Ag, const float* __restrict__ Bg,
-                                              const float* __restrict__ Hg, const float* __restrict__ x0g,
-                                              float* __restrict__ ws, float* __restrict__ out) {
+__global__ void __launch_bounds__(1024) kXeval(const float* __restrict__ Ag, const float* __restrict__ Bg,
+                                               const float* __restrict__ Hg, const float* __restrict__ x0g,
+                                               float* __restrict__ ws, float* __restrict__ out) {
   __shared__ float Atil[64*LDM];
-  __shared__ float Bs[512], BTs[512], BRis[512], Ris[64];
+  __shared__ float BRis[512], Ris[64];
   __shared__ float Hx[512], Bt[512], G[512];
   __shared__ float xv[64], xt[64], xk[64], pk[64], bu[64];
-  __shared__ float ks[4][64], e8v[8], w8[8], uu8[8], red[256];
+  __shared__ float ks[4][64], e8v[8], w8[8], uu8[8], red[1024];
   const int t = threadIdx.x;
   const float* Ps = ws + O_PS;
   const float* xg = ws + O_XG;
   const float* Ug = out + O_U2o;
-  for (int o = t; o < 512; o += 256) { Bs[o] = Bg[o]; BTs[o] = ws[O_BT + o]; BRis[o] = ws[O_BRI + o]; }
+  if (t < 512) BRis[t] = ws[O_BRI + t];
   if (t < 64) { Ris[t] = ws[O_RI + t]; xv[t] = x0g[t]; }
   __syncthreads();
 
@@ -689,27 +639,33 @@
     interpIW(tau, NTS - 2, ix, wx);
     if (t < 64) xk[t] = (1.0f - wx) * xg[ix*64 + t] + wx * xg[(ix+1)*64 + t];
     __syncthreads();
-    mv64_blend(pk, Ps + (size_t)i*4096, Ps + (size_t)(i+1)*4096, 1.0f - w, w, xk, red);
-    if (t < 8) {
-      float s = 0.f;
-      #pragma unroll
-      for (int m = 0; m < 64; ++m) s += BTs[t*64 + m] * pk[m];
-      e8v[t] = s;
-    }
+    mvGb(pk, Ps + (size_t)i*4096, Ps + (size_t)(i+1)*4096, 1.0f - w, w, xk, red);
+    if (t < 512) {
+      const int o = t; float s = 0.f;
+      #pragma unroll 8
+      for (int n = 0; n < 64; ++n) s += ws[O_H1T + n*512 + o] * xk[n];
+      Hx[o] = s; Bt[o] = Bg[o] + s;
+    } else {
+      const int o = t - 512; float s = 0.f;
+      #pragma unroll 8
+      for (int m = 0; m < 64; ++m) s += Hg[m*512 + o] * pk[m];
+      G[o] = s;
+    }
+    __syncthreads();
+    { const int wv = t >> 6, m = t & 63;
+      if (wv < 8) { const float rr = wred64(ws[O_BT + wv*64 + m] * pk[m]); if (m == 0) e8v[wv] = rr; } }
     __syncthreads();
     if (t < 8) {
       float s = 0.f;
       #pragma unroll
       for (int l = 0; l < 8; ++l) s += Ris[t*8 + l] * e8v[l];
       w8[t] = s;
-    }
-    for (int o = t; o < 512; o += 256) {
-      const float hx = dot64g(&ws[O_H1 + o*64], xk);
-      Hx[o] = hx; Bt[o] = Bs[o] + hx;
-      G[o]  = dot64g(&ws[O_H2 + o*64], pk);
-    }
-    __syncthreads();
-    EW_FOR(I, J, IJ, {
+    } else if (t < 16) {
+      const int p = t - 8;
+      uu8[p] = (1.0f - wx) * Ug[ix*8 + p] + wx * Ug[(ix+1)*8 + p];
+    }
+    __syncthreads();
+    EW4(I, J, IJ, {
       const float4 h0 = *(const float4*)&Hg[I*512 + J*8];
       const float4 h1 = *(const float4*)&Hg[I*512 + J*8 + 4];
       Atil[IJ] = h0.x*w8[0]+h0.y*w8[1]+h0.z*w8[2]+h0.w*w8[3]
@@ -718,21 +674,13 @@
     __syncthreads();
     mmNT<8, 8, 8, LDM, 1>(Atil, BRis, G);
     __syncthreads();
-    EW_FOR(I, J, IJ, { Atil[IJ] = Ag[I*64 + J] - 0.5f*Atil[IJ]; });
-    if (t < 8) uu8[t] = (1.0f - wx) * Ug[ix*8 + t] + wx * Ug[(ix+1)*8 + t];
-    __syncthreads();
+    EW4(I, J, IJ, { Atil[IJ] = Ag[I*64 + J] - 0.5f*Atil[IJ]; });
     if (t < 64) {
       float s = 0.f;
       #pragma unroll
       for (int l = 0; l < 8; ++l) s += Bt[t*8 + l] * uu8[l];
       bu[t] = s;
     }
-    __syncthreads();
-  };
-
-  auto fieldE = [&](const float* src, float* kout) {
-    mv64(kout, Atil, LDM, src, red);
-    if (t < 64) kout[t] += bu[t];
     __syncthreads();
   };
 
@@ -744,7 +692,9 @@
     for (int st = 0; st < 4; ++st) {
       if (st != 2) build(tj + ((st == 0) ? 0.0f : (st == 3) ? DT : 0.01f));
       const float* src = (st == 0) ? xv : xt;
-      fieldE(src, ks[st]);
+      mvL(ks[st], Atil, src, red);
+      if (t < 64) ks[st][t] += bu[t];
+      __syncthreads();
       if (t < 64 && st < 3) xt[t] = xv[t] + (st == 2 ? DT : 0.01f) * ks[st][t];
       __syncthreads();
     }
@@ -768,12 +718,12 @@
   (void)in_sizes; (void)n_in; (void)out_size; (void)ws_size;
 
   kPrepA<<<1, 64, 0, stream>>>(R, B, ws);
-  kPrepB<<<96, 256, 0, stream>>>(H, ws, out);
-  kP<<<1, 256, 0, stream>>>(F, Q, A, ws, ws + O_PS);
-  kX0<<<1, 256, 0, stream>>>(A, x0, out);
-  kXgrid<<<1, 256, 0, stream>>>(A, B, x0, ws, out);
-  kXk1<<<1, 256, 0, stream>>>(A, B, H, x0, ws);
-  kPk1<<<1, 256, 0, stream>>>(F, A, B, H, ws);
+  kPrepB<<<64, 256, 0, stream>>>(H, ws, out);
+  kP<<<1, 1024, 0, stream>>>(F, Q, A, ws, ws + O_PS);
+  kX0<<<1, 1024, 0, stream>>>(A, x0, out);
+  kXgrid<<<1, 1024, 0, stream>>>(A, B, x0, ws, out);
+  kXk1<<<1, 1024, 0, stream>>>(A, B, H, x0, ws);
+  kPk1<<<1, 1024, 0, stream>>>(F, A, B, H, ws);
   kUgrid<<<NTS, 256, 0, stream>>>(ws, out);
-  kXeval<<<1, 256, 0, stream>>>(A, B, H, x0, ws, out);
-}
+  kXeval<<<1, 1024, 0, stream>>>(A, B, H, x0, ws, out);
+}
```

Result: faster. 184.3 ms (-19.7%).
